# Performance work log

Hardware: AMD Instinct MI355X
Metric: run time of the kernel (lower is better)

The kernel has to match this reference:

```python
import jax, jax.numpy as jnp
import numpy as np

B, T, H = 8192, 24, 1024


def setup_inputs() -> dict:
    key = jax.random.key(0)
    ks = jax.random.split(key, 16)
    n = lambda k, shp, s=1.0: (jax.random.normal(k, shp, dtype=jnp.float32) * s)
    return {
        "x": n(ks[0], (B, T, 1)),
        "h1_0": n(ks[1], (B, H), 0.02),
        "c1_0": n(ks[2], (B, H), 0.02),
        "h2_0": n(ks[3], (B, H), 0.02),
        "c2_0": n(ks[4], (B, H), 0.02),
        "W_ih1": n(ks[5], (4 * H, 1), 0.05),
        "W_hh1": n(ks[6], (4 * H, H), 0.02),
        "b_ih1": n(ks[7], (4 * H,), 0.02),
        "b_hh1": n(ks[8], (4 * H,), 0.02),
        "W_ih2": n(ks[9], (4 * H, H), 0.02),
        "W_hh2": n(ks[10], (4 * H, H), 0.02),
        "b_ih2": n(ks[11], (4 * H,), 0.02),
        "b_hh2": n(ks[12], (4 * H,), 0.02),
        "W_out": n(ks[13], (2, H), 0.02),
        "b_out": jnp.array([0.2, -0.2], dtype=jnp.float32),
    }


def _lstm_cell(x_t, h, c, W_ih, W_hh, b_ih, b_hh):
    # PyTorch LSTMCell: gates ordered (i, f, g, o)
    gates = x_t @ W_ih.T + b_ih + h @ W_hh.T + b_hh  # [B, 4H]
    i, f, g, o = jnp.split(gates, 4, axis=-1)
    c_new = jax.nn.sigmoid(f) * c + jax.nn.sigmoid(i) * jnp.tanh(g)
    h_new = jax.nn.sigmoid(o) * jnp.tanh(c_new)
    return h_new, c_new


def reference(x, h1_0, c1_0, h2_0, c2_0,
              W_ih1, W_hh1, b_ih1, b_hh1,
              W_ih2, W_hh2, b_ih2, b_hh2,
              W_out, b_out):
    xs = jnp.transpose(x, (1, 0, 2))  # [T, B, 1]

    def step(carry, x_t):
        h1, c1, h2, c2 = carry
        h1, c1 = _lstm_cell(x_t, h1, c1, W_ih1, W_hh1, b_ih1, b_hh1)
        h2, c2 = _lstm_cell(h1, h2, c2, W_ih2, W_hh2, b_ih2, b_hh2)
        return (h1, c1, h2, c2), None

    (h1, c1, h2, c2), _ = jax.lax.scan(step, (h1_0, c1_0, h2_0, c2_0), xs)
    return h2 @ W_out.T + b_out  # [B, 2]
```

## Files before the change

### kernel.cpp

```cpp
#include <hip/hip_runtime.h>
#include <hip/hip_bf16.h>
#include <stdint.h>

#define B_SZ 8192
#define T_SZ 24
#define H_SZ 1024
#define G4   4096

typedef __attribute__((ext_vector_type(8))) short bf16x8;
typedef __attribute__((ext_vector_type(4))) float f32x4;

#define DSR(dst, base, imm) \
    asm volatile("ds_read_b128 %0, %1 offset:" #imm : "=v"(dst) : "v"(base))

__device__ __forceinline__ int perm_old(int p) {
    int gate = (p >> 4) & 3;
    int unit = ((p >> 6) << 4) | (p & 15);
    return gate * 1024 + unit;
}

__device__ __forceinline__ float fast_sigmoid(float x) {
    return 1.f / (1.f + __expf(-x));
}
__device__ __forceinline__ float fast_tanh(float x) {
    float ax = __builtin_fabsf(x);
    float e  = __expf(2.f * ax);
    float r  = 1.f - 2.f / (e + 1.f);
    return __builtin_copysignf(r, x);
}

__global__ void k_prep_w1(const float* __restrict__ Whh1, __hip_bfloat16* __restrict__ dst) {
    int i = blockIdx.x * blockDim.x + threadIdx.x;
    int p = i >> 10, k = i & 1023;
    dst[i] = __float2bfloat16(Whh1[(size_t)perm_old(p) * 1024 + k]);
}

__global__ void k_prep_w2(const float* __restrict__ Wih2, const float* __restrict__ Whh2,
                          __hip_bfloat16* __restrict__ dst) {
    int i = blockIdx.x * blockDim.x + threadIdx.x;
    int p = i >> 11, k = i & 2047;
    int old = perm_old(p);
    float v = (k < 1024) ? Wih2[(size_t)old * 1024 + k] : Whh2[(size_t)old * 1024 + (k - 1024)];
    dst[i] = __float2bfloat16(v);
}

__global__ void k_prep_vec(const float* __restrict__ bih1, const float* __restrict__ bhh1,
                           const float* __restrict__ bih2, const float* __restrict__ bhh2,
                           const float* __restrict__ Wih1,
                           float* __restrict__ b1p, float* __restrict__ b2p,
                           float* __restrict__ w1p) {
    int p = blockIdx.x * blockDim.x + threadIdx.x;
    if (p >= G4) return;
    int old = perm_old(p);
    b1p[p] = bih1[old] + bhh1[old];
    b2p[p] = bih2[old] + bhh2[old];
    w1p[p] = Wih1[old];
}

__global__ void k_xT(const float* __restrict__ x, float* __restrict__ xT) {
    int i = blockIdx.x * blockDim.x + threadIdx.x;
    if (i >= B_SZ * T_SZ) return;
    int b = i / T_SZ, t = i % T_SZ;
    xT[t * B_SZ + b] = x[i];
}

__global__ void k_init_state(const float* __restrict__ h1_0, const float* __restrict__ c1_0,
                             const float* __restrict__ h2_0, const float* __restrict__ c2_0,
                             __hip_bfloat16* __restrict__ A2_0, __hip_bfloat16* __restrict__ A2_1,
                             float* __restrict__ c1, float* __restrict__ c2) {
    int i = blockIdx.x * blockDim.x + threadIdx.x;
    if (i >= B_SZ * H_SZ) return;
    int b = i >> 10, j = i & 1023;
    A2_1[(size_t)b * 2048 + j]        = __float2bfloat16(h1_0[i]);
    A2_0[(size_t)b * 2048 + 1024 + j] = __float2bfloat16(h2_0[i]);
    c1[i] = c1_0[i];
    c2[i] = c2_0[i];
}

#define BM 256
#define BN 256
#define BK 64

template<int LAYER>
__global__ __launch_bounds__(512, 2)
void k_gemm_cell(const __hip_bfloat16* __restrict__ A, int lda,
                 const __hip_bfloat16* __restrict__ Bw, int ldb, int K,
                 const float* __restrict__ biasp, const float* __restrict__ wih1p,
                 const float* __restrict__ xT, int t,
                 float* __restrict__ c, __hip_bfloat16* __restrict__ hout) {
    __shared__ short As[2][BM][BK];
    __shared__ short Bs[2][BN][BK];
    const int tid  = threadIdx.x;
    const int lane = tid & 63;
    const int wid  = tid >> 6;

    const int bid = blockIdx.x;
    const int xcd = bid & 7;
    const int i   = bid >> 3;
    const int ml  = (i & 7) | ((i >> 5) << 3);
    const int nl  = (i >> 3) & 3;
    const int m0  = ((xcd & 1) * 16 + ml) * BM;
    const int n0  = ((xcd >> 1) * 4 + nl) * BN;

    const int wm = wid >> 2;
    const int wn = wid & 3;
    const int fr = lane & 15;
    const int kg = lane >> 4;

    const __hip_bfloat16* Abase = A  + (size_t)m0 * lda;
    const __hip_bfloat16* Bbase = Bw + (size_t)n0 * ldb;

    f32x4 acc[8][4];
#pragma unroll
    for (int ii = 0; ii < 8; ++ii)
#pragma unroll
        for (int j = 0; j < 4; ++j) acc[ii][j] = (f32x4)0.f;

    const int lr8 = lane >> 3;
    const int cr  = lane & 7;
    const int scol = (cr ^ lr8) << 3;
    int lr0_u1[2], lr0_u2[2], lr0_u3[2], lr0_u4[2];
#pragma unroll
    for (int j = 0; j < 2; ++j) {
        int rr0 = (wid * 2 + j) * 8;
        lr0_u1[j] = (rr0 < 64) ? rr0 : rr0 + 64;
        lr0_u2[j] = (rr0 < 64) ? rr0 + 64 : rr0 + 128;
        lr0_u3[j] = ((rr0 >> 5) << 6) + (rr0 & 31);
        lr0_u4[j] = ((rr0 >> 5) << 6) + 32 + (rr0 & 31);
    }
    const __hip_bfloat16* gu1[2]; const __hip_bfloat16* gu2[2];
    const __hip_bfloat16* gu3[2]; const __hip_bfloat16* gu4[2];
#pragma unroll
    for (int j = 0; j < 2; ++j) {
        gu1[j] = Abase + (size_t)(lr0_u1[j] + lr8) * lda + scol;
        gu2[j] = Abase + (size_t)(lr0_u2[j] + lr8) * lda + scol;
        gu3[j] = Bbase + (size_t)(lr0_u3[j] + lr8) * ldb + scol;
        gu4[j] = Bbase + (size_t)(lr0_u4[j] + lr8) * ldb + scol;
    }
    short* const As0p = &As[0][0][0];
    short* const Bs0p = &Bs[0][0][0];

    auto st8 = [&](const __hip_bfloat16*& gp, short* dst) {
        __builtin_amdgcn_global_load_lds(
            (const __attribute__((address_space(1))) void*)gp,
            (__attribute__((address_space(3))) void*)dst, 16, 0, 0);
        gp += BK;
    };
    auto stage_u1 = [&](int buf) {
#pragma unroll
        for (int j = 0; j < 2; ++j) st8(gu1[j], As0p + buf * 16384 + lr0_u1[j] * 64);
    };
    auto stage_u2 = [&](int buf) {
#pragma unroll
        for (int j = 0; j < 2; ++j) st8(gu2[j], As0p + buf * 16384 + lr0_u2[j] * 64);
    };
    auto stage_u3 = [&](int buf) {
#pragma unroll
        for (int j = 0; j < 2; ++j) st8(gu3[j], Bs0p + buf * 16384 + lr0_u3[j] * 64);
    };
    auto stage_u4 = [&](int buf) {
#pragma unroll
        for (int j = 0; j < 2; ++j) st8(gu4[j], Bs0p + buf * 16384 + lr0_u4[j] * 64);
    };

    const unsigned asb = (unsigned)(uintptr_t)(__attribute__((address_space(3))) short*)As0p;
    const unsigned bsb = (unsigned)(uintptr_t)(__attribute__((address_space(3))) short*)Bs0p;
    const unsigned aoffB = (unsigned)((wm * 128 + fr) * 64) * 2;
    const unsigned boffB = (unsigned)((wn * 64 + fr) * 64) * 2;
    const unsigned ck0B  = (unsigned)((kg ^ (fr & 7)) << 3) * 2;
    const unsigned ck1B  = (unsigned)(((4 + kg) ^ (fr & 7)) << 3) * 2;

    const int NK = K >> 6;

    bf16x8 a0[4][2], a1[4][2], b0[2][2], b1[2][2];

    stage_u1(0); stage_u3(0); stage_u2(0); stage_u4(0);
    stage_u3(1); stage_u1(1);
    asm volatile("s_waitcnt vmcnt(4)" ::: "memory");
    __builtin_amdgcn_s_barrier();
    {
        const unsigned bA0 = asb + aoffB + ck0B;
        const unsigned bA1 = asb + aoffB + ck1B;
        const unsigned bB0 = bsb + boffB + ck0B;
        const unsigned bB1 = bsb + boffB + ck1B;
        DSR(b0[0][0], bB0, 0);    DSR(b0[0][1], bB1, 0);
        DSR(b0[1][0], bB0, 2048); DSR(b0[1][1], bB1, 2048);
        DSR(a0[0][0], bA0, 0);    DSR(a0[0][1], bA1, 0);
        DSR(a0[1][0], bA0, 2048); DSR(a0[1][1], bA1, 2048);
        DSR(a0[2][0], bA0, 4096); DSR(a0[2][1], bA1, 4096);
        DSR(a0[3][0], bA0, 6144); DSR(a0[3][1], bA1, 6144);
    }

    for (int kt = 0; kt < NK; ++kt) {
        const int buf = kt & 1;
        const unsigned bo  = (unsigned)buf * 32768u;
        const unsigned nbo = bo ^ 32768u;
        const unsigned bA0 = asb + bo + aoffB + ck0B;
        const unsigned bA1 = asb + bo + aoffB + ck1B;
        const unsigned bB0 = bsb + bo + boffB + ck0B;
        const unsigned bB1 = bsb + bo + boffB + ck1B;
        const unsigned nA0 = asb + nbo + aoffB + ck0B;
        const unsigned nA1 = asb + nbo + aoffB + ck1B;
        const unsigned nB0 = bsb + nbo + boffB + ck0B;
        const unsigned nB1 = bsb + nbo + boffB + ck1B;

        DSR(b1[0][0], bB0, 4096); DSR(b1[0][1], bB1, 4096);
        DSR(b1[1][0], bB0, 6144); DSR(b1[1][1], bB1, 6144);
        if (kt + 1 < NK) { stage_u4(buf ^ 1); stage_u2(buf ^ 1); }
        __builtin_amdgcn_s_barrier();
        asm volatile("s_waitcnt lgkmcnt(4)" ::: "memory");
        __builtin_amdgcn_sched_barrier(0);
        __builtin_amdgcn_s_setprio(1);
#pragma unroll
        for (int ks = 0; ks < 2; ++ks)
#pragma unroll
            for (int m = 0; m < 4; ++m)
#pragma unroll
                for (int n = 0; n < 2; ++n)
                    acc[m][n] = __builtin_amdgcn_mfma_f32_16x16x32_bf16(a0[m][ks], b0[n][ks], acc[m][n], 0, 0, 0);
        __builtin_amdgcn_s_setprio(0);
        __builtin_amdgcn_s_barrier();

        DSR(a1[0][0], bA0, 8192);  DSR(a1[0][1], bA1, 8192);
        DSR(a1[1][0], bA0, 10240); DSR(a1[1][1], bA1, 10240);
        DSR(a1[2][0], bA0, 12288); DSR(a1[2][1], bA1, 12288);
        DSR(a1[3][0], bA0, 14336); DSR(a1[3][1], bA1, 14336);
        __builtin_amdgcn_s_barrier();
        asm volatile("s_waitcnt lgkmcnt(8)" ::: "memory");
        __builtin_amdgcn_sched_barrier(0);
        __builtin_amdgcn_s_setprio(1);
#pragma unroll
        for (int ks = 0; ks < 2; ++ks)
#pragma unroll
            for (int m = 0; m < 4; ++m)
#pragma unroll
                for (int n = 0; n < 2; ++n)
                    acc[m][2 + n] = __builtin_amdgcn_mfma_f32_16x16x32_bf16(a0[m][ks], b1[n][ks], acc[m][2 + n], 0, 0, 0);
        __builtin_amdgcn_s_setprio(0);
        asm volatile("s_waitcnt vmcnt(4)" ::: "memory");
        __builtin_amdgcn_s_barrier();

        if (kt + 2 < NK) { stage_u3(buf); stage_u1(buf); }
        __builtin_amdgcn_s_barrier();
        asm volatile("s_waitcnt lgkmcnt(0)" ::: "memory");
        __builtin_amdgcn_sched_barrier(0);
        __builtin_amdgcn_s_setprio(1);
#pragma unroll
        for (int ks = 0; ks < 2; ++ks)
#pragma unroll
            for (int m = 0; m < 4; ++m)
#pragma unroll
                for (int n = 0; n < 2; ++n)
                    acc[4 + m][2 + n] = __builtin_amdgcn_mfma_f32_16x16x32_bf16(a1[m][ks], b1[n][ks], acc[4 + m][2 + n], 0, 0, 0);
        __builtin_amdgcn_s_setprio(0);
        __builtin_amdgcn_s_barrier();

        __builtin_amdgcn_s_setprio(1);
#pragma unroll
        for (int ks = 0; ks < 2; ++ks)
#pragma unroll
            for (int m = 0; m < 4; ++m)
#pragma unroll
                for (int n = 0; n < 2; ++n)
                    acc[4 + m][n] = __builtin_amdgcn_mfma_f32_16x16x32_bf16(a1[m][ks], b0[n][ks], acc[4 + m][n], 0, 0, 0);
        __builtin_amdgcn_s_setprio(0);
        __builtin_amdgcn_sched_barrier(0);
        if (kt + 1 < NK) {
            DSR(b0[0][0], nB0, 0);    DSR(b0[0][1], nB1, 0);
            DSR(b0[1][0], nB0, 2048); DSR(b0[1][1], nB1, 2048);
            DSR(a0[0][0], nA0, 0);    DSR(a0[0][1], nA1, 0);
            DSR(a0[1][0], nA0, 2048); DSR(a0[1][1], nA1, 2048);
            DSR(a0[2][0], nA0, 4096); DSR(a0[2][1], nA1, 4096);
            DSR(a0[3][0], nA0, 6144); DSR(a0[3][1], nA1, 6144);
        }
        asm volatile("s_waitcnt vmcnt(4)" ::: "memory");
        __builtin_amdgcn_s_barrier();
    }

    float biasv[4], xwv[4];
#pragma unroll
    for (int n = 0; n < 4; ++n) {
        int col = n0 + wn * 64 + n * 16 + fr;
        biasv[n] = biasp[col];
        if (LAYER == 1) xwv[n] = wih1p[col];
    }
    const int u = ((n0 >> 6) + wn) * 16 + fr;

#pragma unroll
    for (int m = 0; m < 8; ++m) {
        int rbase = m0 + wm * 128 + m * 16 + (lane >> 4) * 4;
#pragma unroll
        for (int j = 0; j < 4; ++j) {
            int b = rbase + j;
            float gi = acc[m][0][j] + biasv[0];
            float gf = acc[m][1][j] + biasv[1];
            float gg = acc[m][2][j] + biasv[2];
            float go = acc[m][3][j] + biasv[3];
            if (LAYER == 1) {
                float xv = xT[t * B_SZ + b];
                gi += xv * xwv[0];
                gf += xv * xwv[1];
                gg += xv * xwv[2];
                go += xv * xwv[3];
            }
            float si = fast_sigmoid(gi);
            float sf = fast_sigmoid(gf);
            float so = fast_sigmoid(go);
            float tg = fast_tanh(gg);
            size_t ci = (size_t)b * H_SZ + u;
            float cn = sf * c[ci] + si * tg;
            c[ci] = cn;
            hout[(size_t)b * 2048 + u] = __float2bfloat16(so * fast_tanh(cn));
        }
    }
}

__global__ __launch_bounds__(256)
void k_out(const __hip_bfloat16* __restrict__ h2base, const float* __restrict__ Wout,
           const float* __restrict__ bout, float* __restrict__ out) {
    int gw   = (blockIdx.x * blockDim.x + threadIdx.x) >> 6;
    int lane = threadIdx.x & 63;
    if (gw >= B_SZ) return;
    const __hip_bfloat16* h = h2base + (size_t)gw * 2048;
    float a0 = 0.f, a1 = 0.f;
#pragma unroll
    for (int k = lane; k < 1024; k += 64) {
        float hv = __bfloat162float(h[k]);
        a0 += hv * Wout[k];
        a1 += hv * Wout[1024 + k];
    }
    for (int off = 32; off; off >>= 1) {
        a0 += __shfl_down(a0, off);
        a1 += __shfl_down(a1, off);
    }
    if (lane == 0) {
        out[gw * 2 + 0] = a0 + bout[0];
        out[gw * 2 + 1] = a1 + bout[1];
    }
}

extern "C" void kernel_launch(void* const* d_in, const int* in_sizes, int n_in,
                              void* d_out, int out_size, void* d_ws, size_t ws_size,
                              hipStream_t stream) {
    const float* x    = (const float*)d_in[0];
    const float* h1_0 = (const float*)d_in[1];
    const float* c1_0 = (const float*)d_in[2];
    const float* h2_0 = (const float*)d_in[3];
    const float* c2_0 = (const float*)d_in[4];
    const float* Wih1 = (const float*)d_in[5];
    const float* Whh1 = (const float*)d_in[6];
    const float* bih1 = (const float*)d_in[7];
    const float* bhh1 = (const float*)d_in[8];
    const float* Wih2 = (const float*)d_in[9];
    const float* Whh2 = (const float*)d_in[10];
    const float* bih2 = (const float*)d_in[11];
    const float* bhh2 = (const float*)d_in[12];
    const float* Wout = (const float*)d_in[13];
    const float* bout = (const float*)d_in[14];
    float* out = (float*)d_out;
    (void)in_sizes; (void)n_in; (void)out_size; (void)ws_size;

    uint8_t* ws = (uint8_t*)d_ws;
    size_t off = 0;
    auto alloc = [&](size_t bytes) { void* p = ws + off; off += (bytes + 255) & ~(size_t)255; return p; };
    __hip_bfloat16* A2_0  = (__hip_bfloat16*)alloc((size_t)B_SZ * 2048 * 2);
    __hip_bfloat16* A2_1  = (__hip_bfloat16*)alloc((size_t)B_SZ * 2048 * 2);
    float*          c1    = (float*)alloc((size_t)B_SZ * H_SZ * 4);
    float*          c2    = (float*)alloc((size_t)B_SZ * H_SZ * 4);
    __hip_bfloat16* Whh1p = (__hip_bfloat16*)alloc((size_t)G4 * H_SZ * 2);
    __hip_bfloat16* Wcat2p= (__hip_bfloat16*)alloc((size_t)G4 * 2048 * 2);
    float*          bias1p= (float*)alloc(G4 * 4);
    float*          bias2p= (float*)alloc(G4 * 4);
    float*          wih1p = (float*)alloc(G4 * 4);
    float*          xT    = (float*)alloc((size_t)T_SZ * B_SZ * 4);

    __hip_bfloat16* A2[2] = { A2_0, A2_1 };

    k_prep_w1<<<(G4 * H_SZ + 255) / 256, 256, 0, stream>>>(Whh1, Whh1p);
    k_prep_w2<<<(G4 * 2048 + 255) / 256, 256, 0, stream>>>(Wih2, Whh2, Wcat2p);
    k_prep_vec<<<(G4 + 255) / 256, 256, 0, stream>>>(bih1, bhh1, bih2, bhh2, Wih1,
                                                     bias1p, bias2p, wih1p);
    k_xT<<<(B_SZ * T_SZ + 255) / 256, 256, 0, stream>>>(x, xT);
    k_init_state<<<(B_SZ * H_SZ + 255) / 256, 256, 0, stream>>>(h1_0, c1_0, h2_0, c2_0,
                                                                A2_0, A2_1, c1, c2);

    const int gemm_blocks = (B_SZ / BM) * (G4 / BN);

    for (int t = 0; t < T_SZ; ++t) {
        __hip_bfloat16* Pprev = A2[(t + 1) & 1];
        __hip_bfloat16* Pt    = A2[t & 1];
        k_gemm_cell<1><<<gemm_blocks, 512, 0, stream>>>(
            (const __hip_bfloat16*)Pprev, 2048, Whh1p, 1024, 1024,
            bias1p, wih1p, xT, t, c1, Pt);
        k_gemm_cell<2><<<gemm_blocks, 512, 0, stream>>>(
            (const __hip_bfloat16*)Pt, 2048, Wcat2p, 2048, 2048,
            bias2p, nullptr, nullptr, 0, c2, A2[(t + 1) & 1] + 1024);
    }
    k_out<<<(B_SZ * 64 + 255) / 256, 256, 0, stream>>>(A2_0 + 1024, Wout, bout, out);
}
```

Baseline: 5.198 ms.

## Replace workgroup barriers in GEMM main loop with LDS flag producer/consumer polling

The GEMM k-loop's fine-grained s_barrier schedule is replaced by per-buffer shared-memory counters. Each wave signals with LDS atomics when its global-to-LDS loads have landed or its fragment reads are done, and spins with s_sleep until the counters reach the expected value. All LDS fragment reads for a stage are now issued up front, followed by all 32 MFMAs, and the next tile is staged after that. The aim is to let waves drift apart instead of lock-stepping on barriers. In exchange it gives up the previous interleaving of loads with MFMA phases and adds spin-polling overhead and atomic traffic.

```diff
diff --git a/kernel.cpp b/kernel.cpp
--- a/kernel.cpp
+++ b/kernel.cpp
@@ -90,6 +90,7 @@
                  float* __restrict__ c, __hip_bfloat16* __restrict__ hout) {
     __shared__ short As[2][BM][BK];
     __shared__ short Bs[2][BN][BK];
+    __shared__ int   sync_f[4];
     const int tid  = threadIdx.x;
     const int lane = tid & 63;
     const int wid  = tid >> 6;
@@ -110,6 +111,9 @@
     const __hip_bfloat16* Abase = A  + (size_t)m0 * lda;
     const __hip_bfloat16* Bbase = Bw + (size_t)n0 * ldb;
 
+    if (tid == 0) { sync_f[0] = 0; sync_f[1] = 0; sync_f[2] = 0; sync_f[3] = 0; }
+    __syncthreads();
+
     f32x4 acc[8][4];
 #pragma unroll
     for (int ii = 0; ii < 8; ++ii)
@@ -146,21 +150,24 @@
             (__attribute__((address_space(3))) void*)dst, 16, 0, 0);
         gp += BK;
     };
-    auto stage_u1 = [&](int buf) {
+    auto stage_all = [&](int buf) {
 #pragma unroll
         for (int j = 0; j < 2; ++j) st8(gu1[j], As0p + buf * 16384 + lr0_u1[j] * 64);
+#pragma unroll
+        for (int j = 0; j < 2; ++j) st8(gu2[j], As0p + buf * 16384 + lr0_u2[j] * 64);
+#pragma unroll
+        for (int j = 0; j < 2; ++j) st8(gu3[j], Bs0p + buf * 16384 + lr0_u3[j] * 64);
+#pragma unroll
+        for (int j = 0; j < 2; ++j) st8(gu4[j], Bs0p + buf * 16384 + lr0_u4[j] * 64);
     };
-    auto stage_u2 = [&](int buf) {
-#pragma unroll
-        for (int j = 0; j < 2; ++j) st8(gu2[j], As0p + buf * 16384 + lr0_u2[j] * 64);
+
+    auto poll = [&](int idx, int target) {
+        volatile int* p = (volatile int*)&sync_f[idx];
+        while (*p < target) __builtin_amdgcn_s_sleep(2);
+        asm volatile("" ::: "memory");
     };
-    auto stage_u3 = [&](int buf) {
-#pragma unroll
-        for (int j = 0; j < 2; ++j) st8(gu3[j], Bs0p + buf * 16384 + lr0_u3[j] * 64);
-    };
-    auto stage_u4 = [&](int buf) {
-#pragma unroll
-        for (int j = 0; j < 2; ++j) st8(gu4[j], Bs0p + buf * 16384 + lr0_u4[j] * 64);
+    auto sig = [&](int idx) {
+        if (lane == 0) atomicAdd(&sync_f[idx], 1);
     };
 
     const unsigned asb = (unsigned)(uintptr_t)(__attribute__((address_space(3))) short*)As0p;
@@ -174,61 +181,47 @@
 
     bf16x8 a0[4][2], a1[4][2], b0[2][2], b1[2][2];
 
-    stage_u1(0); stage_u3(0); stage_u2(0); stage_u4(0);
-    stage_u3(1); stage_u1(1);
-    asm volatile("s_waitcnt vmcnt(4)" ::: "memory");
-    __builtin_amdgcn_s_barrier();
-    {
-        const unsigned bA0 = asb + aoffB + ck0B;
-        const unsigned bA1 = asb + aoffB + ck1B;
-        const unsigned bB0 = bsb + boffB + ck0B;
-        const unsigned bB1 = bsb + boffB + ck1B;
-        DSR(b0[0][0], bB0, 0);    DSR(b0[0][1], bB1, 0);
-        DSR(b0[1][0], bB0, 2048); DSR(b0[1][1], bB1, 2048);
-        DSR(a0[0][0], bA0, 0);    DSR(a0[0][1], bA1, 0);
-        DSR(a0[1][0], bA0, 2048); DSR(a0[1][1], bA1, 2048);
-        DSR(a0[2][0], bA0, 4096); DSR(a0[2][1], bA1, 4096);
-        DSR(a0[3][0], bA0, 6144); DSR(a0[3][1], bA1, 6144);
-    }
+    stage_all(0);
+    stage_all(1);
+    asm volatile("s_waitcnt vmcnt(8)" ::: "memory");
+    sig(0);
 
     for (int kt = 0; kt < NK; ++kt) {
-        const int buf = kt & 1;
-        const unsigned bo  = (unsigned)buf * 32768u;
-        const unsigned nbo = bo ^ 32768u;
+        const int s  = kt & 1;
+        const int gt = 8 * ((kt >> 1) + 1);
+
+        poll(s, gt);
+
+        const unsigned bo  = (unsigned)s * 32768u;
         const unsigned bA0 = asb + bo + aoffB + ck0B;
         const unsigned bA1 = asb + bo + aoffB + ck1B;
         const unsigned bB0 = bsb + bo + boffB + ck0B;
         const unsigned bB1 = bsb + bo + boffB + ck1B;
-        const unsigned nA0 = asb + nbo + aoffB + ck0B;
-        const unsigned nA1 = asb + nbo + aoffB + ck1B;
-        const unsigned nB0 = bsb + nbo + boffB + ck0B;
-        const unsigned nB1 = bsb + nbo + boffB + ck1B;
-
-        DSR(b1[0][0], bB0, 4096); DSR(b1[0][1], bB1, 4096);
-        DSR(b1[1][0], bB0, 6144); DSR(b1[1][1], bB1, 6144);
-        if (kt + 1 < NK) { stage_u4(buf ^ 1); stage_u2(buf ^ 1); }
-        __builtin_amdgcn_s_barrier();
-        asm volatile("s_waitcnt lgkmcnt(4)" ::: "memory");
-        __builtin_amdgcn_sched_barrier(0);
-        __builtin_amdgcn_s_setprio(1);
-#pragma unroll
-        for (int ks = 0; ks < 2; ++ks)
-#pragma unroll
-            for (int m = 0; m < 4; ++m)
-#pragma unroll
-                for (int n = 0; n < 2; ++n)
-                    acc[m][n] = __builtin_amdgcn_mfma_f32_16x16x32_bf16(a0[m][ks], b0[n][ks], acc[m][n], 0, 0, 0);
-        __builtin_amdgcn_s_setprio(0);
-        __builtin_amdgcn_s_barrier();
-
+
+        DSR(a0[0][0], bA0, 0);     DSR(a0[0][1], bA1, 0);
+        DSR(a0[1][0], bA0, 2048);  DSR(a0[1][1], bA1, 2048);
+        DSR(a0[2][0], bA0, 4096);  DSR(a0[2][1], bA1, 4096);
+        DSR(a0[3][0], bA0, 6144);  DSR(a0[3][1], bA1, 6144);
+        DSR(b0[0][0], bB0, 0);     DSR(b0[0][1], bB1, 0);
+        DSR(b0[1][0], bB0, 2048);  DSR(b0[1][1], bB1, 2048);
+        DSR(b1[0][0], bB0, 4096);  DSR(b1[0][1], bB1, 4096);
+        DSR(b1[1][0], bB0, 6144);  DSR(b1[1][1], bB1, 6144);
         DSR(a1[0][0], bA0, 8192);  DSR(a1[0][1], bA1, 8192);
         DSR(a1[1][0], bA0, 10240); DSR(a1[1][1], bA1, 10240);
         DSR(a1[2][0], bA0, 12288); DSR(a1[2][1], bA1, 12288);
         DSR(a1[3][0], bA0, 14336); DSR(a1[3][1], bA1, 14336);
-        __builtin_amdgcn_s_barrier();
-        asm volatile("s_waitcnt lgkmcnt(8)" ::: "memory");
+        asm volatile("s_waitcnt lgkmcnt(0)" ::: "memory");
         __builtin_amdgcn_sched_barrier(0);
+        sig(2 + s);
+
         __builtin_amdgcn_s_setprio(1);
+#pragma unroll
+        for (int ks = 0; ks < 2; ++ks)
+#pragma unroll
+            for (int m = 0; m < 4; ++m)
+#pragma unroll
+                for (int n = 0; n < 2; ++n)
+                    acc[m][n] = __builtin_amdgcn_mfma_f32_16x16x32_bf16(a0[m][ks], b0[n][ks], acc[m][n], 0, 0, 0);
 #pragma unroll
         for (int ks = 0; ks < 2; ++ks)
 #pragma unroll
@@ -236,15 +229,13 @@
 #pragma unroll
                 for (int n = 0; n < 2; ++n)
                     acc[m][2 + n] = __builtin_amdgcn_mfma_f32_16x16x32_bf16(a0[m][ks], b1[n][ks], acc[m][2 + n], 0, 0, 0);
-        __builtin_amdgcn_s_setprio(0);
-        asm volatile("s_waitcnt vmcnt(4)" ::: "memory");
-        __builtin_amdgcn_s_barrier();
-
-        if (kt + 2 < NK) { stage_u3(buf); stage_u1(buf); }
-        __builtin_amdgcn_s_barrier();
-        asm volatile("s_waitcnt lgkmcnt(0)" ::: "memory");
-        __builtin_amdgcn_sched_barrier(0);
-        __builtin_amdgcn_s_setprio(1);
+#pragma unroll
+        for (int ks = 0; ks < 2; ++ks)
+#pragma unroll
+            for (int m = 0; m < 4; ++m)
+#pragma unroll
+                for (int n = 0; n < 2; ++n)
+                    acc[4 + m][n] = __builtin_amdgcn_mfma_f32_16x16x32_bf16(a1[m][ks], b0[n][ks], acc[4 + m][n], 0, 0, 0);
 #pragma unroll
         for (int ks = 0; ks < 2; ++ks)
 #pragma unroll
@@ -253,28 +244,16 @@
                 for (int n = 0; n < 2; ++n)
                     acc[4 + m][2 + n] = __builtin_amdgcn_mfma_f32_16x16x32_bf16(a1[m][ks], b1[n][ks], acc[4 + m][2 + n], 0, 0, 0);
         __builtin_amdgcn_s_setprio(0);
-        __builtin_amdgcn_s_barrier();
-
-        __builtin_amdgcn_s_setprio(1);
-#pragma unroll
-        for (int ks = 0; ks < 2; ++ks)
-#pragma unroll
-            for (int m = 0; m < 4; ++m)
-#pragma unroll
-                for (int n = 0; n < 2; ++n)
-                    acc[4 + m][n] = __builtin_amdgcn_mfma_f32_16x16x32_bf16(a1[m][ks], b0[n][ks], acc[4 + m][n], 0, 0, 0);
-        __builtin_amdgcn_s_setprio(0);
-        __builtin_amdgcn_sched_barrier(0);
-        if (kt + 1 < NK) {
-            DSR(b0[0][0], nB0, 0);    DSR(b0[0][1], nB1, 0);
-            DSR(b0[1][0], nB0, 2048); DSR(b0[1][1], nB1, 2048);
-            DSR(a0[0][0], nA0, 0);    DSR(a0[0][1], nA1, 0);
-            DSR(a0[1][0], nA0, 2048); DSR(a0[1][1], nA1, 2048);
-            DSR(a0[2][0], nA0, 4096); DSR(a0[2][1], nA1, 4096);
-            DSR(a0[3][0], nA0, 6144); DSR(a0[3][1], nA1, 6144);
+
+        if (kt + 2 < NK) {
+            poll(2 + s, gt);
+            stage_all(s);
+            asm volatile("s_waitcnt vmcnt(8)" ::: "memory");
+            sig((kt + 1) & 1);
+        } else if (kt + 1 < NK) {
+            asm volatile("s_waitcnt vmcnt(0)" ::: "memory");
+            sig((kt + 1) & 1);
         }
-        asm volatile("s_waitcnt vmcnt(4)" ::: "memory");
-        __builtin_amdgcn_s_barrier();
     }
 
     float biasv[4], xwv[4];
```

After: 5.726 ms. 1.1x slower.
